# Performance work log

Hardware: AMD Instinct MI355X
Metric: run time of the kernel (lower is better)

## Reference

```python
import jax, jax.numpy as jnp
import numpy as np

B = 2048
DIMS = [4096, 8192, 8192, 4096]
SPARSITY = 1e-4


def setup_inputs() -> dict:
    key = jax.random.key(0)
    ks = jax.random.split(key, 10)
    x = jax.random.normal(ks[0], (B, DIMS[0]), dtype=jnp.float32)
    inp = {"x": x}
    for i in range(3):
        fan_in, fan_out = DIMS[i], DIMS[i + 1]
        # xavier_uniform_ for tanh
        limit = float(np.sqrt(6.0 / (fan_in + fan_out)))
        W = jax.random.uniform(ks[1 + 3 * i], (fan_out, fan_in),
                               dtype=jnp.float32, minval=-limit, maxval=limit)
        b = jax.random.uniform(ks[2 + 3 * i], (fan_out,), dtype=jnp.float32,
                               minval=-1.0 / np.sqrt(fan_in), maxval=1.0 / np.sqrt(fan_in))
        m = jax.random.bernoulli(ks[3 + 3 * i], p=SPARSITY, shape=(fan_out, fan_in))
        inp[f"W{i+1}"] = W
        inp[f"b{i+1}"] = b
        inp[f"m{i+1}"] = m
    return inp


def reference(x, W1, b1, m1, W2, b2, m2, W3, b3, m3):
    # Each layer: mask weight, dense linear (y = x @ (W*m)^T + b), tanh except last.
    h = jnp.tanh(x @ (W1 * m1).T + b1)        # [B, 8192]
    h = jnp.tanh(h @ (W2 * m2).T + b2)        # [B, 8192]
    out = h @ (W3 * m3).T + b3                # [B, 4096]
    return out
```

## Files before the change

### kernel.cpp

```cpp
#include <hip/hip_runtime.h>
#include <hip/hip_bf16.h>
#include <stdint.h>

#define CAP 32

static constexpr int BATCH = 2048;
static constexpr int D0 = 4096;
static constexpr int D1 = 8192;
static constexpr int D2 = 8192;
static constexpr int D3 = 4096;
static constexpr int ROWS_PAD = 8192;

static constexpr size_t PREFIX_BYTES = 16u << 20;

static constexpr size_t OFF_DET  = 0;
static constexpr size_t OFF_CNT  = 256;
static constexpr size_t OFF_REFD = OFF_CNT + 3ull*ROWS_PAD*4;
static constexpr size_t OFF_TB   = OFF_REFD + 2ull*ROWS_PAD*4;
static constexpr size_t OFF_RK   = OFF_TB + 2ull*ROWS_PAD*4;
static constexpr size_t OFF_RW   = OFF_RK + 3ull*ROWS_PAD*CAP*4;
static constexpr size_t OFF_XT   = OFF_RW + 3ull*ROWS_PAD*CAP*4;
static constexpr size_t OFF_H1   = OFF_XT + 33554432ull;
static constexpr size_t OFF_H2   = OFF_H1 + 67108864ull;
static constexpr size_t WS_BIG   = OFF_H2 + 67108864ull;
static constexpr size_t ZERO_BYTES = OFF_TB;

__global__ void detect_kernel(const uint8_t* __restrict__ m, unsigned* __restrict__ det) {
    const uint4* p = (const uint4*)m;
    const int n16 = (int)(PREFIX_BYTES / 16);
    unsigned c123 = 0, c4 = 0;
    for (int i = blockIdx.x * blockDim.x + threadIdx.x; i < n16; i += gridDim.x * blockDim.x) {
        uint4 q = p[i];
        if ((q.x | q.y | q.z | q.w) == 0u) continue;
        unsigned w[4] = {q.x, q.y, q.z, q.w};
        for (int t = 0; t < 4; ++t) {
            unsigned v = w[t];
            if (!v) continue;
            for (int bb = 0; bb < 4; ++bb) {
                if ((v >> (8 * bb)) & 0xFFu) {
                    int posmod8 = ((t * 4 + bb) & 7);
                    if (posmod8 & 3) c123++;
                    else if (posmod8 == 4) c4++;
                }
            }
        }
    }
    if (c123) atomicAdd(&det[0], c123);
    if (c4)   atomicAdd(&det[1], c4);
}

__device__ __forceinline__ int decide_mode(const unsigned* det) {
    unsigned c123 = det[0], c4 = det[1];
    if (c123 > 1050u) return 0;
    if (c123 > 400u)  return 1;
    return (c4 > 80u) ? 1 : 2;
}

__global__ void extract_kernel(const void* __restrict__ mask, const float* __restrict__ W,
                               int fan_in,
                               int* __restrict__ cnt, int* __restrict__ rowk,
                               float* __restrict__ roww, const unsigned* __restrict__ det,
                               int* __restrict__ refd_prev) {
    const int row = blockIdx.x;
    const int mode = decide_mode(det);

    __shared__ int lcnt;
    __shared__ int lk[CAP];
    if (threadIdx.x == 0) lcnt = 0;
    __syncthreads();

    auto push = [&](int k) {
        int pos = atomicAdd(&lcnt, 1);
        if (pos < CAP) lk[pos] = k;
    };

    if (mode == 0) {
        const uint4* p = (const uint4*)((const uint8_t*)mask + (size_t)row * fan_in);
        const int nch = fan_in / 16;
        for (int ci = threadIdx.x; ci < nch; ci += blockDim.x) {
            uint4 q = p[ci];
            if ((q.x | q.y | q.z | q.w) == 0u) continue;
            unsigned w[4] = {q.x, q.y, q.z, q.w};
            int base = ci * 16;
            for (int t = 0; t < 4; ++t) {
                unsigned v = w[t];
                if (!v) continue;
                for (int bb = 0; bb < 4; ++bb)
                    if ((v >> (8 * bb)) & 0xFFu) push(base + t * 4 + bb);
            }
        }
    } else if (mode == 1) {
        const int4* p = (const int4*)((const int*)mask + (size_t)row * fan_in);
        const int nch = fan_in / 4;
        for (int ci = threadIdx.x; ci < nch; ci += blockDim.x) {
            int4 q = p[ci];
            if ((q.x | q.y | q.z | q.w) == 0) continue;
            int base = ci * 4;
            if (q.x) push(base + 0);
            if (q.y) push(base + 1);
            if (q.z) push(base + 2);
            if (q.w) push(base + 3);
        }
    } else {
        const longlong2* p = (const longlong2*)((const long long*)mask + (size_t)row * fan_in);
        const int nch = fan_in / 2;
        for (int ci = threadIdx.x; ci < nch; ci += blockDim.x) {
            longlong2 q = p[ci];
            if ((q.x | q.y) == 0ll) continue;
            int base = ci * 2;
            if (q.x) push(base + 0);
            if (q.y) push(base + 1);
        }
    }
    __syncthreads();

    if (threadIdx.x == 0) {
        int c = lcnt;
        if (c > CAP) c = CAP;
        for (int a = 1; a < c; ++a) {
            int v = lk[a];
            int b = a - 1;
            while (b >= 0 && lk[b] > v) { lk[b + 1] = lk[b]; --b; }
            lk[b + 1] = v;
        }
        cnt[row] = c;
        for (int a = 0; a < c; ++a) {
            int k = lk[a];
            rowk[(size_t)row * CAP + a] = k;
            roww[(size_t)row * CAP + a] = W[(size_t)row * fan_in + k];
            if (refd_prev) atomicOr(&refd_prev[k], 1);
        }
    }
}

__global__ void tb_kernel(const float* __restrict__ b1, const float* __restrict__ b2,
                          float* __restrict__ tb1, float* __restrict__ tb2) {
    int i = blockIdx.x * blockDim.x + threadIdx.x;
    if (i < D1) tb1[i] = tanhf(b1[i]);
    else if (i < D1 + D2) tb2[i - D1] = tanhf(b2[i - D1]);
}

__global__ void transpose_kernel(const float* __restrict__ in, float* __restrict__ out,
                                 int R, int C) {
    __shared__ float tile[32][33];
    int c0 = blockIdx.x * 32, r0 = blockIdx.y * 32;
    for (int i = threadIdx.y; i < 32; i += 8)
        tile[i][threadIdx.x] = in[(size_t)(r0 + i) * C + c0 + threadIdx.x];
    __syncthreads();
    for (int i = threadIdx.y; i < 32; i += 8)
        out[(size_t)(c0 + i) * R + r0 + threadIdx.x] = tile[threadIdx.x][i];
}

template<bool TANH, bool HAS_TB, bool CHECK>
__global__ void layer_kernel(const float* __restrict__ inT,
                             const float* __restrict__ bias,
                             const float* __restrict__ tb_in,
                             const int* __restrict__ cnt_in,
                             const int* __restrict__ cnt,
                             const int* __restrict__ rowk,
                             const float* __restrict__ roww,
                             const int* __restrict__ refd,
                             float* __restrict__ outT) {
    const int j = blockIdx.x;
    const int c = cnt[j];
    if (CHECK) { if (c == 0 || refd[j] == 0) return; }

    const int*   kk = rowk + (size_t)j * CAP;
    const float* ww = roww + (size_t)j * CAP;

    float base = bias[j];
    if (HAS_TB) {
        for (int e = 0; e < c; ++e) {
            int k = kk[e];
            if (cnt_in[k] == 0) base += ww[e] * tb_in[k];
        }
    }

    const int l = threadIdx.x;
    float4 acc0 = make_float4(base, base, base, base);
    float4 acc1 = acc0;

    for (int e = 0; e < c; ++e) {
        int k = kk[e];
        if (HAS_TB && cnt_in[k] == 0) continue;
        const float w = ww[e];
        const float* row = inT + (size_t)k * BATCH;
        float4 v0 = *(const float4*)(row + l * 4);
        float4 v1 = *(const float4*)(row + 1024 + l * 4);
        acc0.x += w * v0.x; acc0.y += w * v0.y; acc0.z += w * v0.z; acc0.w += w * v0.w;
        acc1.x += w * v1.x; acc1.y += w * v1.y; acc1.z += w * v1.z; acc1.w += w * v1.w;
    }

    if (TANH) {
        acc0.x = tanhf(acc0.x); acc0.y = tanhf(acc0.y);
        acc0.z = tanhf(acc0.z); acc0.w = tanhf(acc0.w);
        acc1.x = tanhf(acc1.x); acc1.y = tanhf(acc1.y);
        acc1.z = tanhf(acc1.z); acc1.w = tanhf(acc1.w);
    }

    float* orow = outT + (size_t)j * BATCH;
    *(float4*)(orow + l * 4) = acc0;
    *(float4*)(orow + 1024 + l * 4) = acc1;
}

__global__ void out_kernel(const float* __restrict__ x,
                           const float* __restrict__ b1, const float* __restrict__ b2,
                           const float* __restrict__ b3,
                           const int* __restrict__ c1, const int* __restrict__ k1,
                           const float* __restrict__ w1,
                           const int* __restrict__ c2, const int* __restrict__ k2,
                           const float* __restrict__ w2,
                           const int* __restrict__ c3, const int* __restrict__ k3,
                           const float* __restrict__ w3,
                           float* __restrict__ out) {
    int idx = blockIdx.x * blockDim.x + threadIdx.x;
    if (idx >= BATCH * D3) return;
    int b = idx >> 12;
    int j = idx & 4095;

    float acc = b3[j];
    int c = c3[j];
    for (int e = 0; e < c; ++e) {
        int kk2 = k3[(size_t)j * CAP + e];
        float a2 = b2[kk2];
        int cc2 = c2[kk2];
        for (int e2 = 0; e2 < cc2; ++e2) {
            int kk1 = k2[(size_t)kk2 * CAP + e2];
            float a1 = b1[kk1];
            int cc1 = c1[kk1];
            for (int e1 = 0; e1 < cc1; ++e1) {
                int kk0 = k1[(size_t)kk1 * CAP + e1];
                a1 += w1[(size_t)kk1 * CAP + e1] * x[(size_t)b * D0 + kk0];
            }
            a2 += w2[(size_t)kk2 * CAP + e2] * tanhf(a1);
        }
        acc += w3[(size_t)j * CAP + e] * tanhf(a2);
    }
    out[idx] = acc;
}

extern "C" void kernel_launch(void* const* d_in, const int* in_sizes, int n_in,
                              void* d_out, int out_size, void* d_ws, size_t ws_size,
                              hipStream_t stream) {
    const float* x  = (const float*)d_in[0];
    const float* W1 = (const float*)d_in[1];
    const float* b1 = (const float*)d_in[2];
    const void*  m1 = d_in[3];
    const float* W2 = (const float*)d_in[4];
    const float* b2 = (const float*)d_in[5];
    const void*  m2 = d_in[6];
    const float* W3 = (const float*)d_in[7];
    const float* b3 = (const float*)d_in[8];
    const void*  m3 = d_in[9];

    uint8_t* ws = (uint8_t*)d_ws;
    unsigned* det = (unsigned*)(ws + OFF_DET);
    int* cnt1 = (int*)(ws + OFF_CNT);
    int* cnt2 = cnt1 + ROWS_PAD;
    int* cnt3 = cnt2 + ROWS_PAD;
    int* refd1 = (int*)(ws + OFF_REFD);
    int* refd2 = refd1 + ROWS_PAD;
    float* tb1 = (float*)(ws + OFF_TB);
    float* tb2 = tb1 + ROWS_PAD;
    int* rk1 = (int*)(ws + OFF_RK);
    int* rk2 = rk1 + (size_t)ROWS_PAD * CAP;
    int* rk3 = rk2 + (size_t)ROWS_PAD * CAP;
    float* rw1 = (float*)(ws + OFF_RW);
    float* rw2 = rw1 + (size_t)ROWS_PAD * CAP;
    float* rw3 = rw2 + (size_t)ROWS_PAD * CAP;
    float* xT   = (float*)(ws + OFF_XT);
    float* outT = (float*)(ws + OFF_XT);
    float* h1T  = (float*)(ws + OFF_H1);
    float* h2T  = (float*)(ws + OFF_H2);

    hipMemsetAsync(ws, 0, ZERO_BYTES, stream);

    detect_kernel<<<1024, 256, 0, stream>>>((const uint8_t*)m1, det);

    extract_kernel<<<D1, 256, 0, stream>>>(m1, W1, D0, cnt1, rk1, rw1, det, nullptr);
    extract_kernel<<<D2, 256, 0, stream>>>(m2, W2, D1, cnt2, rk2, rw2, det, refd1);
    extract_kernel<<<D3, 256, 0, stream>>>(m3, W3, D2, cnt3, rk3, rw3, det, refd2);

    if (ws_size >= WS_BIG) {
        tb_kernel<<<(D1 + D2) / 256, 256, 0, stream>>>(b1, b2, tb1, tb2);

        transpose_kernel<<<dim3(D0 / 32, BATCH / 32), dim3(32, 8), 0, stream>>>(x, xT, BATCH, D0);

        layer_kernel<true, false, true><<<D1, 256, 0, stream>>>(
            xT, b1, nullptr, nullptr, cnt1, rk1, rw1, refd1, h1T);
        layer_kernel<true, true, true><<<D2, 256, 0, stream>>>(
            h1T, b2, tb1, cnt1, cnt2, rk2, rw2, refd2, h2T);
        layer_kernel<false, true, false><<<D3, 256, 0, stream>>>(
            h2T, b3, tb2, cnt2, cnt3, rk3, rw3, nullptr, outT);

        transpose_kernel<<<dim3(BATCH / 32, D3 / 32), dim3(32, 8), 0, stream>>>(
            outT, (float*)d_out, D3, BATCH);
    } else {
        out_kernel<<<(BATCH * D3 + 255) / 256, 256, 0, stream>>>(
            x, b1, b2, b3,
            cnt1, rk1, rw1,
            cnt2, rk2, rw2,
            cnt3, rk3, rw3,
            (float*)d_out);
    }
}
```

Before: 192.6 us.

## Merge extract launches, skip unused x columns, fuse layer-3 with output transpose

Folds the three per-layer mask extraction launches and the tanh-bias kernel into one launch. The x transpose now writes only the columns some layer-1 row references, tracked in a new xneed array that layer-1 extraction sets. Layer 3 is fused with the final transpose through a shared-memory tile, so the intermediate outT buffer is gone. This cuts launch count and write traffic. The cost is that each block-row in l3t reads gathered h2T rows with less coalescing.

```diff
diff --git a/kernel.cpp b/kernel.cpp
--- a/kernel.cpp
+++ b/kernel.cpp
@@ -13,17 +13,18 @@
 
 static constexpr size_t PREFIX_BYTES = 16u << 20;
 
-static constexpr size_t OFF_DET  = 0;
-static constexpr size_t OFF_CNT  = 256;
-static constexpr size_t OFF_REFD = OFF_CNT + 3ull*ROWS_PAD*4;
-static constexpr size_t OFF_TB   = OFF_REFD + 2ull*ROWS_PAD*4;
-static constexpr size_t OFF_RK   = OFF_TB + 2ull*ROWS_PAD*4;
-static constexpr size_t OFF_RW   = OFF_RK + 3ull*ROWS_PAD*CAP*4;
-static constexpr size_t OFF_XT   = OFF_RW + 3ull*ROWS_PAD*CAP*4;
-static constexpr size_t OFF_H1   = OFF_XT + 33554432ull;
-static constexpr size_t OFF_H2   = OFF_H1 + 67108864ull;
-static constexpr size_t WS_BIG   = OFF_H2 + 67108864ull;
-static constexpr size_t ZERO_BYTES = OFF_TB;
+static constexpr size_t OFF_DET   = 0;
+static constexpr size_t OFF_CNT   = 256;
+static constexpr size_t OFF_REFD  = OFF_CNT + 3ull*ROWS_PAD*4;
+static constexpr size_t OFF_XNEED = OFF_REFD + 2ull*ROWS_PAD*4;
+static constexpr size_t ZERO_BYTES= OFF_XNEED + (size_t)D0*4;
+static constexpr size_t OFF_TB    = ZERO_BYTES;
+static constexpr size_t OFF_RK    = OFF_TB + 2ull*ROWS_PAD*4;
+static constexpr size_t OFF_RW    = OFF_RK + 3ull*ROWS_PAD*CAP*4;
+static constexpr size_t OFF_XT    = OFF_RW + 3ull*ROWS_PAD*CAP*4;
+static constexpr size_t OFF_H1    = OFF_XT + 33554432ull;
+static constexpr size_t OFF_H2    = OFF_H1 + 67108864ull;
+static constexpr size_t WS_BIG    = OFF_H2 + 67108864ull;
 
 __global__ void detect_kernel(const uint8_t* __restrict__ m, unsigned* __restrict__ det) {
     const uint4* p = (const uint4*)m;
@@ -56,14 +57,10 @@
     return (c4 > 80u) ? 1 : 2;
 }
 
-__global__ void extract_kernel(const void* __restrict__ mask, const float* __restrict__ W,
-                               int fan_in,
-                               int* __restrict__ cnt, int* __restrict__ rowk,
-                               float* __restrict__ roww, const unsigned* __restrict__ det,
-                               int* __restrict__ refd_prev) {
-    const int row = blockIdx.x;
-    const int mode = decide_mode(det);
-
+__device__ __forceinline__ void extract_row(const void* mask, const float* W,
+                                            int fan_in, int row, int mode,
+                                            int* cnt, int* rowk, float* roww,
+                                            int* refd_prev) {
     __shared__ int lcnt;
     __shared__ int lk[CAP];
     if (threadIdx.x == 0) lcnt = 0;
@@ -133,25 +130,45 @@
     }
 }
 
-__global__ void tb_kernel(const float* __restrict__ b1, const float* __restrict__ b2,
-                          float* __restrict__ tb1, float* __restrict__ tb2) {
-    int i = blockIdx.x * blockDim.x + threadIdx.x;
-    if (i < D1) tb1[i] = tanhf(b1[i]);
-    else if (i < D1 + D2) tb2[i - D1] = tanhf(b2[i - D1]);
-}
-
-__global__ void transpose_kernel(const float* __restrict__ in, float* __restrict__ out,
-                                 int R, int C) {
+__global__ void extract_all_kernel(const void* __restrict__ m1, const float* __restrict__ W1,
+                                   const void* __restrict__ m2, const float* __restrict__ W2,
+                                   const void* __restrict__ m3, const float* __restrict__ W3,
+                                   const float* __restrict__ b1, const float* __restrict__ b2,
+                                   const unsigned* __restrict__ det,
+                                   int* __restrict__ cnt1, int* __restrict__ cnt2, int* __restrict__ cnt3,
+                                   int* __restrict__ rk1, int* __restrict__ rk2, int* __restrict__ rk3,
+                                   float* __restrict__ rw1, float* __restrict__ rw2, float* __restrict__ rw3,
+                                   int* __restrict__ refd1, int* __restrict__ refd2,
+                                   int* __restrict__ xneed,
+                                   float* __restrict__ tb1, float* __restrict__ tb2) {
+    const int bid = blockIdx.x;
+    const int mode = decide_mode(det);
+    if (bid < D1) {
+        extract_row(m1, W1, D0, bid, mode, cnt1, rk1, rw1, xneed);
+    } else if (bid < D1 + D2) {
+        extract_row(m2, W2, D1, bid - D1, mode, cnt2, rk2, rw2, refd1);
+    } else if (bid < D1 + D2 + D3) {
+        extract_row(m3, W3, D2, bid - D1 - D2, mode, cnt3, rk3, rw3, refd2);
+    } else {
+        int tid = (bid - (D1 + D2 + D3)) * 256 + threadIdx.x;
+        if (tid < D1) tb1[tid] = tanhf(b1[tid]);
+        else if (tid < D1 + D2) tb2[tid - D1] = tanhf(b2[tid - D1]);
+    }
+}
+
+__global__ void transpose_x_kernel(const float* __restrict__ in, float* __restrict__ out,
+                                   const int* __restrict__ xneed) {
     __shared__ float tile[32][33];
     int c0 = blockIdx.x * 32, r0 = blockIdx.y * 32;
     for (int i = threadIdx.y; i < 32; i += 8)
-        tile[i][threadIdx.x] = in[(size_t)(r0 + i) * C + c0 + threadIdx.x];
+        tile[i][threadIdx.x] = in[(size_t)(r0 + i) * D0 + c0 + threadIdx.x];
     __syncthreads();
     for (int i = threadIdx.y; i < 32; i += 8)
-        out[(size_t)(c0 + i) * R + r0 + threadIdx.x] = tile[threadIdx.x][i];
-}
-
-template<bool TANH, bool HAS_TB, bool CHECK>
+        if (xneed[c0 + i])
+            out[(size_t)(c0 + i) * BATCH + r0 + threadIdx.x] = tile[threadIdx.x][i];
+}
+
+template<bool HAS_TB>
 __global__ void layer_kernel(const float* __restrict__ inT,
                              const float* __restrict__ bias,
                              const float* __restrict__ tb_in,
@@ -163,7 +180,7 @@
                              float* __restrict__ outT) {
     const int j = blockIdx.x;
     const int c = cnt[j];
-    if (CHECK) { if (c == 0 || refd[j] == 0) return; }
+    if (c == 0 || refd[j] == 0) return;
 
     const int*   kk = rowk + (size_t)j * CAP;
     const float* ww = roww + (size_t)j * CAP;
@@ -191,16 +208,45 @@
         acc1.x += w * v1.x; acc1.y += w * v1.y; acc1.z += w * v1.z; acc1.w += w * v1.w;
     }
 
-    if (TANH) {
-        acc0.x = tanhf(acc0.x); acc0.y = tanhf(acc0.y);
-        acc0.z = tanhf(acc0.z); acc0.w = tanhf(acc0.w);
-        acc1.x = tanhf(acc1.x); acc1.y = tanhf(acc1.y);
-        acc1.z = tanhf(acc1.z); acc1.w = tanhf(acc1.w);
-    }
+    acc0.x = tanhf(acc0.x); acc0.y = tanhf(acc0.y);
+    acc0.z = tanhf(acc0.z); acc0.w = tanhf(acc0.w);
+    acc1.x = tanhf(acc1.x); acc1.y = tanhf(acc1.y);
+    acc1.z = tanhf(acc1.z); acc1.w = tanhf(acc1.w);
 
     float* orow = outT + (size_t)j * BATCH;
     *(float4*)(orow + l * 4) = acc0;
     *(float4*)(orow + 1024 + l * 4) = acc1;
+}
+
+__global__ void l3t_kernel(const float* __restrict__ h2T,
+                           const float* __restrict__ b3, const float* __restrict__ tb2,
+                           const int* __restrict__ cnt2,
+                           const int* __restrict__ c3, const int* __restrict__ k3,
+                           const float* __restrict__ w3,
+                           float* __restrict__ out) {
+    __shared__ float tile[32][33];
+    const int j0 = blockIdx.x * 32, b0 = blockIdx.y * 32;
+    const int tx = threadIdx.x, ty = threadIdx.y;
+
+    for (int s = 0; s < 4; ++s) {
+        int jl = ty + 8 * s;
+        int j = j0 + jl;
+        float acc = b3[j];
+        int c = c3[j];
+        const int* kk = k3 + (size_t)j * CAP;
+        const float* ww = w3 + (size_t)j * CAP;
+        for (int e = 0; e < c; ++e) {
+            int k = kk[e];
+            float w = ww[e];
+            acc += w * (cnt2[k] ? h2T[(size_t)k * BATCH + b0 + tx] : tb2[k]);
+        }
+        tile[jl][tx] = acc;
+    }
+    __syncthreads();
+    for (int s = 0; s < 4; ++s) {
+        int bl = ty + 8 * s;
+        out[(size_t)(b0 + bl) * D3 + j0 + tx] = tile[tx][bl];
+    }
 }
 
 __global__ void out_kernel(const float* __restrict__ x,
@@ -260,6 +306,7 @@
     int* cnt3 = cnt2 + ROWS_PAD;
     int* refd1 = (int*)(ws + OFF_REFD);
     int* refd2 = refd1 + ROWS_PAD;
+    int* xneed = (int*)(ws + OFF_XNEED);
     float* tb1 = (float*)(ws + OFF_TB);
     float* tb2 = tb1 + ROWS_PAD;
     int* rk1 = (int*)(ws + OFF_RK);
@@ -268,33 +315,29 @@
     float* rw1 = (float*)(ws + OFF_RW);
     float* rw2 = rw1 + (size_t)ROWS_PAD * CAP;
     float* rw3 = rw2 + (size_t)ROWS_PAD * CAP;
-    float* xT   = (float*)(ws + OFF_XT);
-    float* outT = (float*)(ws + OFF_XT);
-    float* h1T  = (float*)(ws + OFF_H1);
-    float* h2T  = (float*)(ws + OFF_H2);
+    float* xT  = (float*)(ws + OFF_XT);
+    float* h1T = (float*)(ws + OFF_H1);
+    float* h2T = (float*)(ws + OFF_H2);
 
     hipMemsetAsync(ws, 0, ZERO_BYTES, stream);
 
     detect_kernel<<<1024, 256, 0, stream>>>((const uint8_t*)m1, det);
 
-    extract_kernel<<<D1, 256, 0, stream>>>(m1, W1, D0, cnt1, rk1, rw1, det, nullptr);
-    extract_kernel<<<D2, 256, 0, stream>>>(m2, W2, D1, cnt2, rk2, rw2, det, refd1);
-    extract_kernel<<<D3, 256, 0, stream>>>(m3, W3, D2, cnt3, rk3, rw3, det, refd2);
+    const int EX_BLOCKS = D1 + D2 + D3 + (D1 + D2) / 256;
+    extract_all_kernel<<<EX_BLOCKS, 256, 0, stream>>>(
+        m1, W1, m2, W2, m3, W3, b1, b2, det,
+        cnt1, cnt2, cnt3, rk1, rk2, rk3, rw1, rw2, rw3,
+        refd1, refd2, xneed, tb1, tb2);
 
     if (ws_size >= WS_BIG) {
-        tb_kernel<<<(D1 + D2) / 256, 256, 0, stream>>>(b1, b2, tb1, tb2);
-
-        transpose_kernel<<<dim3(D0 / 32, BATCH / 32), dim3(32, 8), 0, stream>>>(x, xT, BATCH, D0);
-
-        layer_kernel<true, false, true><<<D1, 256, 0, stream>>>(
+        transpose_x_kernel<<<dim3(D0 / 32, BATCH / 32), dim3(32, 8), 0, stream>>>(x, xT, xneed);
+
+        layer_kernel<false><<<D1, 256, 0, stream>>>(
             xT, b1, nullptr, nullptr, cnt1, rk1, rw1, refd1, h1T);
-        layer_kernel<true, true, true><<<D2, 256, 0, stream>>>(
+        layer_kernel<true><<<D2, 256, 0, stream>>>(
             h1T, b2, tb1, cnt1, cnt2, rk2, rw2, refd2, h2T);
-        layer_kernel<false, true, false><<<D3, 256, 0, stream>>>(
-            h2T, b3, tb2, cnt2, cnt3, rk3, rw3, nullptr, outT);
-
-        transpose_kernel<<<dim3(BATCH / 32, D3 / 32), dim3(32, 8), 0, stream>>>(
-            outT, (float*)d_out, D3, BATCH);
+        l3t_kernel<<<dim3(D3 / 32, BATCH / 32), dim3(32, 8), 0, stream>>>(
+            h2T, b3, tb2, cnt2, cnt3, rk3, rw3, (float*)d_out);
     } else {
         out_kernel<<<(BATCH * D3 + 255) / 256, 256, 0, stream>>>(
             x, b1, b2, b3,
```

After: 190.2 us. No clear change (-1.3%).
